# Optimization experiments

Measured on AMD Instinct MI355X. Metric: run time of the kernel, lower is better.

The kernel has to match this reference:

```python
import jax, jax.numpy as jnp
import numpy as np

BN_EPS = 1e-5
PAD = 31 // 2  # conv 'same' padding for kernel_size=31


def setup_inputs() -> dict:
    key0 = jax.random.key(0)
    ks = jax.random.split(key0, 12)
    B, T, E, R, A, F, K = 64, 1024, 512, 1024, 128, 32, 31
    return {
        "query": jax.random.normal(ks[0], (B, 1, R), jnp.float32),
        "key": jax.random.normal(ks[1], (B, T, E), jnp.float32),
        "attention_weights_cat": jax.random.uniform(ks[2], (B, 2, T), jnp.float32),
        "mask": jax.random.randint(ks[3], (B, T), 0, 2).astype(bool),
        "Wq": jax.random.normal(ks[4], (R, A), jnp.float32) * 0.03,
        "Wk": jax.random.normal(ks[5], (E, A), jnp.float32) * 0.04,
        "conv_w": jax.random.normal(ks[6], (F, 2, K), jnp.float32) * 0.2,
        "bn_gamma": jnp.ones((F,), jnp.float32),
        "bn_beta": jnp.zeros((F,), jnp.float32),
        "bn_mean": jnp.zeros((F,), jnp.float32),
        "bn_var": jnp.ones((F,), jnp.float32),
        "Wloc": jax.random.normal(ks[7], (F, A), jnp.float32) * 0.1,
        "v": jax.random.normal(ks[8], (A, 1), jnp.float32) * 0.1,
    }


def reference(query, key, attention_weights_cat, mask, Wq, Wk, conv_w,
              bn_gamma, bn_beta, bn_mean, bn_var, Wloc, v):
    # projections: query [B,1,A], key [B,T,A]
    q = query @ Wq
    k = key @ Wk
    # location features: conv1d (no bias) -> relu -> batchnorm (eval stats) -> linear
    loc = jax.lax.conv_general_dilated(
        attention_weights_cat, conv_w, window_strides=(1,),
        padding=[(PAD, PAD)], dimension_numbers=("NCH", "OIH", "NCH"))  # [B,F,T]
    loc = jax.nn.relu(loc)
    inv = jax.lax.rsqrt(bn_var + BN_EPS)
    loc = (loc - bn_mean[None, :, None]) * (inv * bn_gamma)[None, :, None] + bn_beta[None, :, None]
    loc = jnp.swapaxes(loc, 1, 2) @ Wloc  # [B,T,A]
    # additive energies -> masked softmax over time
    energies = (jnp.tanh(q + k + loc) @ v)[..., 0]  # [B,T]
    energies = jnp.where(mask, -jnp.inf, energies)
    attention_weights = jax.nn.softmax(energies, axis=1)
    attention_context = jnp.einsum("bt,bte->be", attention_weights, key)
    return attention_context, attention_weights
```

## Files before the change

kernel.cpp:

```cpp
#include <hip/hip_runtime.h>
#include <hip/hip_bf16.h>
#include <math.h>

#define NB 64
#define NT 1024
#define NE 512
#define NR 1024
#define NA 128
#define NF 32
#define NK 31
#define CPAD 15
#define BN_EPS 1e-5f

typedef __attribute__((ext_vector_type(4))) float f32x4;
typedef __attribute__((ext_vector_type(16))) float f32x16;
typedef __attribute__((ext_vector_type(8))) short bf16x8;
typedef __attribute__((ext_vector_type(8))) unsigned short ushort8v;

#define WS_QPROJ 0
#define WS_ENERG 32768
#define WS_WKHI  294912
#define WS_WKLO  425984
#define WS_WLHI  557056
#define WS_WLLO  565248
#define WS_PART  573440

__device__ __forceinline__ ushort f2bf(float x) {
  union { float f; unsigned u; } v; v.f = x;
  unsigned r = v.u + 0x7fffu + ((v.u >> 16) & 1u);
  return (ushort)(r >> 16);
}
__device__ __forceinline__ float bf2f(ushort h) {
  union { unsigned u; float f; } v; v.u = ((unsigned)h) << 16; return v.f;
}
__device__ __forceinline__ float tanh_fast(float x) {
  float ax = fminf(fabsf(x), 15.f);
  float e = __expf(2.f * ax);
  float r = (e - 1.f) / (e + 1.f);
  return copysignf(r, x);
}

__global__ __launch_bounds__(256) void kprep(
    const float* __restrict__ Wk, const float* __restrict__ Wloc,
    const float* __restrict__ query, const float* __restrict__ Wq,
    ushort* __restrict__ wkhi, ushort* __restrict__ wklo,
    ushort* __restrict__ wlhi, ushort* __restrict__ wllo,
    float* __restrict__ qproj) {
  __shared__ float qs[NR];
  __shared__ float part[128];
  const int blk = blockIdx.x;
  const int tid = threadIdx.x;
  if (blk < 16) {
#pragma unroll
    for (int it = 0; it < 16; ++it) {
      int g = blk * 4096 + it * 256 + tid;
      int j = g & 7, l = (g >> 3) & 63, n = (g >> 9) & 3, kk = g >> 11;
      int k = kk * 16 + (l >> 5) * 8 + j;
      int a = n * 32 + (l & 31);
      float val = Wk[k * NA + a];
      ushort hi = f2bf(val);
      wkhi[g] = hi;
      wklo[g] = f2bf(val - bf2f(hi));
    }
  } else if (blk == 16) {
#pragma unroll
    for (int it = 0; it < 16; ++it) {
      int g = it * 256 + tid;
      int j = g & 7, l = (g >> 3) & 63, n = (g >> 9) & 3, kk = g >> 11;
      int f = kk * 16 + (l >> 5) * 8 + j;
      int a = n * 32 + (l & 31);
      float val = Wloc[f * NA + a];
      ushort hi = f2bf(val);
      wlhi[g] = hi;
      wllo[g] = f2bf(val - bf2f(hi));
    }
  } else {
    const int b = blk - 17;
    for (int i = tid; i < NR; i += 256) qs[i] = query[b * NR + i];
    __syncthreads();
    int a = tid & 127, h = tid >> 7;
    float acc = 0.f;
#pragma unroll 8
    for (int r = h * 512; r < h * 512 + 512; ++r) acc += qs[r] * Wq[r * NA + a];
    if (h) part[a] = acc;
    __syncthreads();
    if (!h) qproj[b * NA + a] = acc + part[a];
  }
}

__global__ __launch_bounds__(256, 2) void ke(
    const float* __restrict__ key, const float* __restrict__ aw,
    const float* __restrict__ conv_w, const float* __restrict__ bn_g,
    const float* __restrict__ bn_b, const float* __restrict__ bn_m,
    const float* __restrict__ bn_v,
    const ushort* __restrict__ wkhi, const ushort* __restrict__ wklo,
    const ushort* __restrict__ wlhi, const ushort* __restrict__ wllo,
    const float* __restrict__ vvec, const float* __restrict__ qproj,
    float* __restrict__ energies) {
  __shared__ ushort khi[128 * 64];
  __shared__ ushort klo[128 * 64];
  __shared__ ushort bhl[8192];
  __shared__ ushort bll[8192];
  __shared__ float x_lds[2][160];
  __shared__ float cw[NF * 2 * NK];
  __shared__ float q_lds[NA], v_lds[NA];

  const int b = blockIdx.x;
  const int t0 = blockIdx.y * 128;
  const int tid = threadIdx.x;
  const int l = tid & 63;
  const int w = tid >> 6;

  for (int i = tid; i < 2 * 158; i += 256) {
    int c = i / 158, p = i - c * 158;
    int t = t0 - CPAD + p;
    x_lds[c][p] = (t >= 0 && t < NT) ? aw[b * 2 * NT + c * NT + t] : 0.f;
  }
  for (int i = tid; i < NF * 2 * NK; i += 256) cw[i] = conv_w[i];
  if (tid < NA) {
    q_lds[tid] = qproj[b * NA + tid];
    v_lds[tid] = vvec[tid];
  }

  f32x16 acc[4];
#pragma unroll
  for (int n = 0; n < 4; ++n)
#pragma unroll
    for (int r = 0; r < 16; ++r) acc[n][r] = 0.f;

  const float* kbase = key + (size_t)b * NT * NE + (size_t)t0 * NE;

  for (int ec = 0; ec < 8; ++ec) {
    __syncthreads();
#pragma unroll
    for (int i = 0; i < 8; ++i) {
      int fi = i * 256 + tid;
      int row = fi >> 4, c4 = fi & 15;
      float4 v4 = *(const float4*)(kbase + (size_t)row * NE + ec * 64 + c4 * 4);
      ushort4 h4, lo4;
      h4.x = f2bf(v4.x); lo4.x = f2bf(v4.x - bf2f(h4.x));
      h4.y = f2bf(v4.y); lo4.y = f2bf(v4.y - bf2f(h4.y));
      h4.z = f2bf(v4.z); lo4.z = f2bf(v4.z - bf2f(h4.z));
      h4.w = f2bf(v4.w); lo4.w = f2bf(v4.w - bf2f(h4.w));
      int byteoff = (row * 128 + c4 * 8) ^ ((row & 7) << 4);
      *(ushort4*)((char*)khi + byteoff) = h4;
      *(ushort4*)((char*)klo + byteoff) = lo4;
    }
    {
      const ushort8v* sh = (const ushort8v*)(wkhi + ec * 8192);
      const ushort8v* sl = (const ushort8v*)(wklo + ec * 8192);
#pragma unroll
      for (int i = 0; i < 4; ++i) {
        int idx = i * 256 + tid;
        ((ushort8v*)bhl)[idx] = sh[idx];
        ((ushort8v*)bll)[idx] = sl[idx];
      }
    }
    __syncthreads();
#pragma unroll
    for (int kk = 0; kk < 4; ++kk) {
      int row = w * 32 + (l & 31);
      int abyte = (row * 128 + kk * 32 + ((l >> 5) * 16)) ^ ((l & 7) << 4);
      bf16x8 ahi = *(bf16x8*)((char*)khi + abyte);
      bf16x8 alo = *(bf16x8*)((char*)klo + abyte);
#pragma unroll
      for (int n = 0; n < 4; ++n) {
        bf16x8 bh = *(bf16x8*)(bhl + ((kk * 4 + n) * 64 + l) * 8);
        bf16x8 bl = *(bf16x8*)(bll + ((kk * 4 + n) * 64 + l) * 8);
        acc[n] = __builtin_amdgcn_mfma_f32_32x32x16_bf16(ahi, bh, acc[n], 0, 0, 0);
        acc[n] = __builtin_amdgcn_mfma_f32_32x32x16_bf16(ahi, bl, acc[n], 0, 0, 0);
        acc[n] = __builtin_amdgcn_mfma_f32_32x32x16_bf16(alo, bh, acc[n], 0, 0, 0);
      }
    }
  }

  __syncthreads();
  {
    const ushort8v* sh = (const ushort8v*)wlhi;
    const ushort8v* sl = (const ushort8v*)wllo;
#pragma unroll
    for (int i = 0; i < 2; ++i) {
      int idx = i * 256 + tid;
      ((ushort8v*)bhl)[idx] = sh[idx];
      ((ushort8v*)bll)[idx] = sl[idx];
    }
  }
  {
    int t = tid & 127, fg = tid >> 7;
    ushort8v fh[2], fl[2];
#pragma unroll
    for (int ff = 0; ff < 16; ++ff) {
      int f = fg * 16 + ff;
      float s = 0.f;
#pragma unroll
      for (int c = 0; c < 2; ++c)
#pragma unroll
        for (int k = 0; k < NK; ++k)
          s += cw[(f * 2 + c) * NK + k] * x_lds[c][t + k];
      s = fmaxf(s, 0.f);
      float scale = rsqrtf(bn_v[f] + BN_EPS) * bn_g[f];
      float bias = bn_b[f] - bn_m[f] * scale;
      s = s * scale + bias;
      ushort hi = f2bf(s);
      ((ushort*)fh)[ff] = hi;
      ((ushort*)fl)[ff] = f2bf(s - bf2f(hi));
    }
    int base0 = (t * 64 + fg * 32) ^ ((t & 7) << 4);
    int base1 = (t * 64 + fg * 32 + 16) ^ ((t & 7) << 4);
    *(ushort8v*)((char*)khi + base0) = fh[0];
    *(ushort8v*)((char*)khi + base1) = fh[1];
    *(ushort8v*)((char*)klo + base0) = fl[0];
    *(ushort8v*)((char*)klo + base1) = fl[1];
  }
  __syncthreads();
#pragma unroll
  for (int kk = 0; kk < 2; ++kk) {
    int row = w * 32 + (l & 31);
    int abyte = (row * 64 + kk * 32 + ((l >> 5) * 16)) ^ ((row & 7) << 4);
    bf16x8 ahi = *(bf16x8*)((char*)khi + abyte);
    bf16x8 alo = *(bf16x8*)((char*)klo + abyte);
#pragma unroll
    for (int n = 0; n < 4; ++n) {
      bf16x8 bh = *(bf16x8*)(bhl + ((kk * 4 + n) * 64 + l) * 8);
      bf16x8 bl = *(bf16x8*)(bll + ((kk * 4 + n) * 64 + l) * 8);
      acc[n] = __builtin_amdgcn_mfma_f32_32x32x16_bf16(ahi, bh, acc[n], 0, 0, 0);
      acc[n] = __builtin_amdgcn_mfma_f32_32x32x16_bf16(ahi, bl, acc[n], 0, 0, 0);
      acc[n] = __builtin_amdgcn_mfma_f32_32x32x16_bf16(alo, bh, acc[n], 0, 0, 0);
    }
  }

  float er[16];
#pragma unroll
  for (int r = 0; r < 16; ++r) er[r] = 0.f;
#pragma unroll
  for (int n = 0; n < 4; ++n) {
    int a = n * 32 + (l & 31);
    float qa = q_lds[a], va = v_lds[a];
#pragma unroll
    for (int r = 0; r < 16; ++r) er[r] += tanh_fast(acc[n][r] + qa) * va;
  }
#pragma unroll
  for (int r = 0; r < 16; ++r) {
    float s = er[r];
    s += __shfl_xor(s, 1, 64);
    s += __shfl_xor(s, 2, 64);
    s += __shfl_xor(s, 4, 64);
    s += __shfl_xor(s, 8, 64);
    s += __shfl_xor(s, 16, 64);
    if ((l & 31) == 0)
      energies[b * NT + t0 + w * 32 + 4 * (l >> 5) + (r & 3) + 8 * (r >> 2)] = s;
  }
}

__global__ __launch_bounds__(256) void ks(const float* __restrict__ energies,
                                          const int* __restrict__ mask,
                                          float* __restrict__ wout) {
  __shared__ float redmax[4];
  __shared__ float redsum[4];
  int b = blockIdx.x;
  int tid = threadIdx.x;
  float vals[4];
  float mx = -INFINITY;
#pragma unroll
  for (int j = 0; j < 4; ++j) {
    int t = tid + j * 256;
    float e = energies[b * NT + t];
    if (mask[b * NT + t] != 0) e = -INFINITY;
    vals[j] = e;
    mx = fmaxf(mx, e);
  }
#pragma unroll
  for (int m = 1; m < 64; m <<= 1) mx = fmaxf(mx, __shfl_xor(mx, m, 64));
  if ((tid & 63) == 0) redmax[tid >> 6] = mx;
  __syncthreads();
  mx = fmaxf(fmaxf(redmax[0], redmax[1]), fmaxf(redmax[2], redmax[3]));
  float s = 0.f;
#pragma unroll
  for (int j = 0; j < 4; ++j) {
    float p = expf(vals[j] - mx);
    vals[j] = p;
    s += p;
  }
#pragma unroll
  for (int m = 1; m < 64; m <<= 1) s += __shfl_xor(s, m, 64);
  if ((tid & 63) == 0) redsum[tid >> 6] = s;
  __syncthreads();
  s = redsum[0] + redsum[1] + redsum[2] + redsum[3];
  float inv = 1.f / s;
#pragma unroll
  for (int j = 0; j < 4; ++j) wout[b * NT + tid + j * 256] = vals[j] * inv;
}

__global__ __launch_bounds__(256) void kc1(const float* __restrict__ key,
                                           const float* __restrict__ wout,
                                           float* __restrict__ part) {
  __shared__ float w_lds[128];
  int b = blockIdx.x, tc = blockIdx.y;
  int tid = threadIdx.x;
  if (tid < 128) w_lds[tid] = wout[b * NT + tc * 128 + tid];
  __syncthreads();
  const float* kp = key + (size_t)b * NT * NE + (size_t)tc * 128 * NE + tid;
  float a0 = 0.f, a1 = 0.f;
#pragma unroll 8
  for (int t = 0; t < 128; ++t) {
    float wv = w_lds[t];
    a0 += wv * kp[(size_t)t * NE];
    a1 += wv * kp[(size_t)t * NE + 256];
  }
  part[(b * 8 + tc) * NE + tid] = a0;
  part[(b * 8 + tc) * NE + tid + 256] = a1;
}

__global__ __launch_bounds__(512) void kc2(const float* __restrict__ part,
                                           float* __restrict__ ctx) {
  int b = blockIdx.x, e = threadIdx.x;
  float s = 0.f;
#pragma unroll
  for (int tc = 0; tc < 8; ++tc) s += part[(b * 8 + tc) * NE + e];
  ctx[b * NE + e] = s;
}

extern "C" void kernel_launch(void* const* d_in, const int* in_sizes, int n_in,
                              void* d_out, int out_size, void* d_ws, size_t ws_size,
                              hipStream_t stream) {
  const float* query  = (const float*)d_in[0];
  const float* key    = (const float*)d_in[1];
  const float* aw     = (const float*)d_in[2];
  const int*   mask   = (const int*)d_in[3];
  const float* Wq     = (const float*)d_in[4];
  const float* Wk     = (const float*)d_in[5];
  const float* conv_w = (const float*)d_in[6];
  const float* bn_g   = (const float*)d_in[7];
  const float* bn_b   = (const float*)d_in[8];
  const float* bn_m   = (const float*)d_in[9];
  const float* bn_v   = (const float*)d_in[10];
  const float* Wloc   = (const float*)d_in[11];
  const float* vvec   = (const float*)d_in[12];

  float* ctx  = (float*)d_out;
  float* wout = (float*)d_out + NB * NE;

  char* ws = (char*)d_ws;
  float*  qproj    = (float*)(ws + WS_QPROJ);
  float*  energies = (float*)(ws + WS_ENERG);
  ushort* wkhi     = (ushort*)(ws + WS_WKHI);
  ushort* wklo     = (ushort*)(ws + WS_WKLO);
  ushort* wlhi     = (ushort*)(ws + WS_WLHI);
  ushort* wllo     = (ushort*)(ws + WS_WLLO);
  float*  partial  = (float*)(ws + WS_PART);

  kprep<<<dim3(17 + NB), dim3(256), 0, stream>>>(Wk, Wloc, query, Wq,
                                                 wkhi, wklo, wlhi, wllo, qproj);
  ke<<<dim3(NB, NT / 128), dim3(256), 0, stream>>>(
      key, aw, conv_w, bn_g, bn_b, bn_m, bn_v,
      wkhi, wklo, wlhi, wllo, vvec, qproj, energies);
  ks<<<dim3(NB), dim3(256), 0, stream>>>(energies, mask, wout);
  kc1<<<dim3(NB, 8), dim3(256), 0, stream>>>(key, wout, partial);
  kc2<<<dim3(NB), dim3(512), 0, stream>>>(partial, ctx);
}
```

Measured before the change: 298.2 us.

## Software-pipeline key tile loads with async LDS B staging; widen context kernel

The energy kernel's main loop is restructured so the next key tile's global loads are issued into registers one iteration ahead. Weight tiles are staged into LDS with global_load_lds, and manual waitcnt plus barriers replace the __syncthreads pairs, aiming to hide global latency behind MFMA work. The context kernel switches to float4 loads with 16 time chunks and an in-block two-way reduction, doubling the number of partials that kc2 sums. The hand-placed waitcnt counts and raw barriers make the synchronisation fragile, and the extra in-flight registers may affect occupancy.

```diff
diff --git a/kernel.cpp b/kernel.cpp
--- a/kernel.cpp
+++ b/kernel.cpp
@@ -39,6 +39,9 @@
   float r = (e - 1.f) / (e + 1.f);
   return copysignf(r, x);
 }
+
+#define FENCE() asm volatile("" ::: "memory")
+#define WAIT_LGKM0() asm volatile("s_waitcnt lgkmcnt(0)" ::: "memory")
 
 __global__ __launch_bounds__(256) void kprep(
     const float* __restrict__ Wk, const float* __restrict__ Wloc,
@@ -85,6 +88,46 @@
     if (h) part[a] = acc;
     __syncthreads();
     if (!h) qproj[b * NA + a] = acc + part[a];
+  }
+}
+
+__device__ __forceinline__ void issue_kr(const float* kbase, int ec, int tid,
+                                         f32x4 kr[8]) {
+#pragma unroll
+  for (int i = 0; i < 8; ++i) {
+    int fi = i * 256 + tid;
+    int row = fi >> 4, c4 = fi & 15;
+    kr[i] = *(const f32x4*)(kbase + (size_t)row * NE + ec * 64 + c4 * 4);
+  }
+}
+
+__device__ __forceinline__ void cw_tile(const f32x4 kr[8], int tid,
+                                        ushort* khi, ushort* klo) {
+#pragma unroll
+  for (int i = 0; i < 8; ++i) {
+    int fi = i * 256 + tid;
+    int row = fi >> 4, c4 = fi & 15;
+    f32x4 v4 = kr[i];
+    ushort4 h4, lo4;
+    h4.x = f2bf(v4.x); lo4.x = f2bf(v4.x - bf2f(h4.x));
+    h4.y = f2bf(v4.y); lo4.y = f2bf(v4.y - bf2f(h4.y));
+    h4.z = f2bf(v4.z); lo4.z = f2bf(v4.z - bf2f(h4.z));
+    h4.w = f2bf(v4.w); lo4.w = f2bf(v4.w - bf2f(h4.w));
+    int byteoff = (row * 128 + c4 * 8) ^ ((row & 7) << 4);
+    *(ushort4*)((char*)khi + byteoff) = h4;
+    *(ushort4*)((char*)klo + byteoff) = lo4;
+  }
+}
+
+__device__ __forceinline__ void stage_B(const ushort* src_base, ushort* lds_base,
+                                        int wv, int lane) {
+#pragma unroll
+  for (int p = 0; p < 4; ++p) {
+    const ushort* g = src_base + wv * 2048 + p * 512 + lane * 8;
+    ushort* d = lds_base + wv * 2048 + p * 512;
+    __builtin_amdgcn_global_load_lds(
+        (const __attribute__((address_space(1))) unsigned int*)g,
+        (__attribute__((address_space(3))) unsigned int*)d, 16, 0, 0);
   }
 }
 
@@ -130,33 +173,20 @@
 
   const float* kbase = key + (size_t)b * NT * NE + (size_t)t0 * NE;
 
+  __syncthreads();
+
+  f32x4 kr[8];
+  issue_kr(kbase, 0, tid, kr);
+  stage_B(wkhi + 0, bhl, w, l);
+  stage_B(wklo + 0, bll, w, l);
+  cw_tile(kr, tid, khi, klo);
+  issue_kr(kbase, 1, tid, kr);
+  asm volatile("s_waitcnt vmcnt(8)" ::: "memory");
+  WAIT_LGKM0();
+  __builtin_amdgcn_s_barrier();
+  FENCE();
+
   for (int ec = 0; ec < 8; ++ec) {
-    __syncthreads();
-#pragma unroll
-    for (int i = 0; i < 8; ++i) {
-      int fi = i * 256 + tid;
-      int row = fi >> 4, c4 = fi & 15;
-      float4 v4 = *(const float4*)(kbase + (size_t)row * NE + ec * 64 + c4 * 4);
-      ushort4 h4, lo4;
-      h4.x = f2bf(v4.x); lo4.x = f2bf(v4.x - bf2f(h4.x));
-      h4.y = f2bf(v4.y); lo4.y = f2bf(v4.y - bf2f(h4.y));
-      h4.z = f2bf(v4.z); lo4.z = f2bf(v4.z - bf2f(h4.z));
-      h4.w = f2bf(v4.w); lo4.w = f2bf(v4.w - bf2f(h4.w));
-      int byteoff = (row * 128 + c4 * 8) ^ ((row & 7) << 4);
-      *(ushort4*)((char*)khi + byteoff) = h4;
-      *(ushort4*)((char*)klo + byteoff) = lo4;
-    }
-    {
-      const ushort8v* sh = (const ushort8v*)(wkhi + ec * 8192);
-      const ushort8v* sl = (const ushort8v*)(wklo + ec * 8192);
-#pragma unroll
-      for (int i = 0; i < 4; ++i) {
-        int idx = i * 256 + tid;
-        ((ushort8v*)bhl)[idx] = sh[idx];
-        ((ushort8v*)bll)[idx] = sl[idx];
-      }
-    }
-    __syncthreads();
 #pragma unroll
     for (int kk = 0; kk < 4; ++kk) {
       int row = w * 32 + (l & 31);
@@ -172,9 +202,26 @@
         acc[n] = __builtin_amdgcn_mfma_f32_32x32x16_bf16(alo, bh, acc[n], 0, 0, 0);
       }
     }
-  }
-
-  __syncthreads();
+    WAIT_LGKM0();
+    __builtin_amdgcn_s_barrier();
+    FENCE();
+    if (ec < 7) {
+      stage_B(wkhi + (ec + 1) * 8192, bhl, w, l);
+      stage_B(wklo + (ec + 1) * 8192, bll, w, l);
+      cw_tile(kr, tid, khi, klo);
+      if (ec < 6) {
+        issue_kr(kbase, ec + 2, tid, kr);
+        asm volatile("s_waitcnt vmcnt(8)" ::: "memory");
+      } else {
+        asm volatile("s_waitcnt vmcnt(0)" ::: "memory");
+      }
+      WAIT_LGKM0();
+      __builtin_amdgcn_s_barrier();
+      FENCE();
+    }
+  }
+
+  FENCE();
   {
     const ushort8v* sh = (const ushort8v*)wlhi;
     const ushort8v* sl = (const ushort8v*)wllo;
@@ -216,7 +263,7 @@
 #pragma unroll
   for (int kk = 0; kk < 2; ++kk) {
     int row = w * 32 + (l & 31);
-    int abyte = (row * 64 + kk * 32 + ((l >> 5) * 16)) ^ ((row & 7) << 4);
+    int abyte = ((row * 64 + kk * 32 + ((l >> 5) * 16))) ^ ((row & 7) << 4);
     bf16x8 ahi = *(bf16x8*)((char*)khi + abyte);
     bf16x8 alo = *(bf16x8*)((char*)klo + abyte);
 #pragma unroll
@@ -294,21 +341,27 @@
 __global__ __launch_bounds__(256) void kc1(const float* __restrict__ key,
                                            const float* __restrict__ wout,
                                            float* __restrict__ part) {
-  __shared__ float w_lds[128];
+  __shared__ float w_lds[64];
+  __shared__ f32x4 red[128];
   int b = blockIdx.x, tc = blockIdx.y;
   int tid = threadIdx.x;
-  if (tid < 128) w_lds[tid] = wout[b * NT + tc * 128 + tid];
-  __syncthreads();
-  const float* kp = key + (size_t)b * NT * NE + (size_t)tc * 128 * NE + tid;
-  float a0 = 0.f, a1 = 0.f;
+  if (tid < 64) w_lds[tid] = wout[b * NT + tc * 64 + tid];
+  __syncthreads();
+  int e4 = (tid & 127) * 4, th = tid >> 7;
+  const float* kp = key + (size_t)b * NT * NE + (size_t)(tc * 64 + th * 32) * NE + e4;
+  f32x4 acc = (f32x4){0.f, 0.f, 0.f, 0.f};
 #pragma unroll 8
-  for (int t = 0; t < 128; ++t) {
-    float wv = w_lds[t];
-    a0 += wv * kp[(size_t)t * NE];
-    a1 += wv * kp[(size_t)t * NE + 256];
-  }
-  part[(b * 8 + tc) * NE + tid] = a0;
-  part[(b * 8 + tc) * NE + tid + 256] = a1;
+  for (int t = 0; t < 32; ++t) {
+    float wv = w_lds[th * 32 + t];
+    f32x4 k4 = *(const f32x4*)(kp + (size_t)t * NE);
+    acc += wv * k4;
+  }
+  if (th) red[tid & 127] = acc;
+  __syncthreads();
+  if (!th) {
+    acc += red[tid];
+    *(f32x4*)&part[((size_t)(b * 16 + tc)) * NE + e4] = acc;
+  }
 }
 
 __global__ __launch_bounds__(512) void kc2(const float* __restrict__ part,
@@ -316,7 +369,7 @@
   int b = blockIdx.x, e = threadIdx.x;
   float s = 0.f;
 #pragma unroll
-  for (int tc = 0; tc < 8; ++tc) s += part[(b * 8 + tc) * NE + e];
+  for (int tc = 0; tc < 16; ++tc) s += part[(b * 16 + tc) * NE + e];
   ctx[b * NE + e] = s;
 }
 
@@ -355,6 +408,6 @@
       key, aw, conv_w, bn_g, bn_b, bn_m, bn_v,
       wkhi, wklo, wlhi, wllo, vvec, qproj, energies);
   ks<<<dim3(NB), dim3(256), 0, stream>>>(energies, mask, wout);
-  kc1<<<dim3(NB, 8), dim3(256), 0, stream>>>(key, wout, partial);
+  kc1<<<dim3(NB, 16), dim3(256), 0, stream>>>(key, wout, partial);
   kc2<<<dim3(NB), dim3(512), 0, stream>>>(partial, ctx);
 }
```

After: 296.4 us. No clear change (-0.6%).
